# Optimization experiments

Measured on AMD Instinct MI355X. Metric: run time of the kernel, lower is better.

The kernel has to match this reference:

```python
import jax, jax.numpy as jnp
import numpy as np

N_QUBITS = 10
DIM = 2 ** N_QUBITS
W_MUL = (2.0 ** 0.5) * 5.0 ** (-0.5)  # he_std * lrmul, use_wscale=True, lrmul=1
MEASURE_QUBIT = 5


def _c(v):
    return v.astype(jnp.complex64)


def _m2(a, b, c, d):
    return jnp.stack([jnp.stack([a, b]), jnp.stack([c, d])])


_ZERO = jnp.zeros((), jnp.complex64)


def _rx(phi):
    c, s = _c(jnp.cos(phi / 2)), _c(jnp.sin(phi / 2))
    return _m2(c, -1j * s, -1j * s, c)


def _ry(phi):
    c, s = _c(jnp.cos(phi / 2)), _c(jnp.sin(phi / 2))
    return _m2(c, -s, s, c)


def _rz(phi):
    c, s = _c(jnp.cos(phi / 2)), _c(jnp.sin(phi / 2))
    return _m2(c - 1j * s, _ZERO, _ZERO, c + 1j * s)


_CNOT = jnp.array([[1, 0, 0, 0], [0, 1, 0, 0], [0, 0, 0, 1], [0, 0, 1, 0]], jnp.complex64)


def _expand(g, n, q):
    # kron(I_{2^q}, g, I_{2^{n-q-k}}) where g acts on qubits q..q+k-1
    k = int(np.log2(g.shape[0]))
    left = jnp.eye(2 ** q, dtype=jnp.complex64)
    right = jnp.eye(2 ** (n - q - k), dtype=jnp.complex64)
    return jnp.kron(left, jnp.kron(g, right))


def _layer_unitary(weight):
    w = weight * W_MUL
    U = jnp.eye(DIM, dtype=jnp.complex64)
    for sign in (1.0, -1.0):
        for q in range(N_QUBITS):
            U = _expand(_rx(sign * w[q]), N_QUBITS, q) @ U
            U = _expand(_ry(sign * w[q + 10]), N_QUBITS, q) @ U
            U = _expand(_rz(sign * w[q + 20]), N_QUBITS, q) @ U
        for q in range(1, N_QUBITS):
            U = _expand(_CNOT, N_QUBITS, q - 1) @ U
    return U


def _measure_affinity(rho, which_q):
    # Tr(rho @ Z_which_q) with Z_q = kron(I, Z, I); Z_q is diagonal
    z = jnp.array([1.0, -1.0], jnp.float32)
    zdiag = jnp.kron(jnp.ones(2 ** which_q, jnp.float32),
                     jnp.kron(z, jnp.ones(2 ** (N_QUBITS - which_q - 1), jnp.float32)))
    return jnp.sum(jnp.diagonal(rho).real * zdiag).astype(jnp.float32)


def setup_inputs() -> dict:
    key = jax.random.key(0)
    k1, k2 = jax.random.split(key)
    x = jax.random.normal(k1, (DIM, DIM), dtype=jnp.float32)
    weight = jax.random.uniform(k2, (30,), dtype=jnp.float32, minval=0.0, maxval=2.0 * np.pi)
    return {"x": x, "weight": weight}


def reference(x, weight):
    E = _layer_unitary(weight)
    rho = (E @ x.astype(jnp.complex64)) @ E.conj().T
    return _measure_affinity(rho, MEASURE_QUBIT)
```

## Files before the change

kernel.cpp:

```cpp
#include <hip/hip_runtime.h>

#define DIM 1024
#define NQ 10

__device__ __forceinline__ float2 cmul(float2 a, float2 b) {
    return make_float2(a.x * b.x - a.y * b.y, a.x * b.y + a.y * b.x);
}
__device__ __forceinline__ float2 cadd(float2 a, float2 b) {
    return make_float2(a.x + b.x, a.y + b.y);
}
__device__ __forceinline__ float2 csub(float2 a, float2 b) {
    return make_float2(a.x - b.x, a.y - b.y);
}
__device__ __forceinline__ float2 cconj(float2 a) { return make_float2(a.x, -a.y); }

__device__ __forceinline__ void mm2(const float2* A, const float2* B, float2* C) {
    C[0] = cadd(cmul(A[0], B[0]), cmul(A[1], B[2]));
    C[1] = cadd(cmul(A[0], B[1]), cmul(A[1], B[3]));
    C[2] = cadd(cmul(A[2], B[0]), cmul(A[3], B[2]));
    C[3] = cadd(cmul(A[2], B[1]), cmul(A[3], B[3]));
}

__device__ __forceinline__ void compute_gates(const float* __restrict__ weight,
                                              float2* G, float2* Msh, int tid) {
    if (tid < NQ) {
        int q = tid;
        const float WM = 0.632455532033676f;
        float px = weight[q]      * WM * 0.5f;
        float py = weight[q + 10] * WM * 0.5f;
        float pz = weight[q + 20] * WM * 0.5f;
        float cx = cosf(px), sx = sinf(px);
        float cy = cosf(py), sy = sinf(py);
        float cz = cosf(pz), sz = sinf(pz);
        {
            float2 Rx[4] = { {cx, 0.f}, {0.f, -sx}, {0.f, -sx}, {cx, 0.f} };
            float2 Ry[4] = { {cy, 0.f}, {-sy, 0.f}, {sy, 0.f}, {cy, 0.f} };
            float2 Rz[4] = { {cz, -sz}, {0.f, 0.f}, {0.f, 0.f}, {cz, sz} };
            float2 T[4], u[4];
            mm2(Ry, Rx, T);
            mm2(Rz, T, u);
            G[q * 4 + 0] = u[0]; G[q * 4 + 1] = u[1];
            G[q * 4 + 2] = u[2]; G[q * 4 + 3] = u[3];
        }
        if (Msh && q < 6) {
            float nsx = -sx, nsy = -sy, nsz = -sz;
            float2 Rx[4] = { {cx, 0.f}, {0.f, -nsx}, {0.f, -nsx}, {cx, 0.f} };
            float2 Ry[4] = { {cy, 0.f}, {-nsy, 0.f}, {nsy, 0.f}, {cy, 0.f} };
            float2 Rz[4] = { {cz, -nsz}, {0.f, 0.f}, {0.f, 0.f}, {cz, nsz} };
            float2 T[4], u2[4];
            mm2(Ry, Rx, T);
            mm2(Rz, T, u2);
            for (int i = 0; i < 2; i++)
                for (int j = 0; j < 2; j++) {
                    float2 v = csub(cmul(cconj(u2[0 * 2 + i]), u2[0 * 2 + j]),
                                    cmul(cconj(u2[1 * 2 + i]), u2[1 * 2 + j]));
                    Msh[q * 4 + i * 2 + j] = v;
                }
        }
    }
}

__global__ __launch_bounds__(512) void pass1(const float* __restrict__ x,
                                             const float* __restrict__ weight,
                                             float2* __restrict__ zt,
                                             float* __restrict__ out) {
    __shared__ float2 G[40];
    __shared__ float2 sh[DIM * 5];
    int tid = threadIdx.x;
    int lane = tid & 63;
    int w = tid >> 6;
    int rl = w >> 1;
    int h = w & 1;
    int r = blockIdx.x * 4 + rl;

    const float* xp = x + r * DIM + (h << 9) + lane;
    float2 v[8];
#pragma unroll
    for (int j = 0; j < 8; j++) v[j] = make_float2(xp[j * 64], 0.f);

    compute_gates(weight, G, nullptr, tid);
    if (blockIdx.x == 0 && tid == 0) out[0] = 0.f;
    __syncthreads();

#pragma unroll
    for (int q = 1; q < 4; q++) {
        float2 u0 = cconj(G[q * 4]),     u1 = cconj(G[q * 4 + 1]);
        float2 u2 = cconj(G[q * 4 + 2]), u3 = cconj(G[q * 4 + 3]);
        const int hb = 1 << (3 - q);
#pragma unroll
        for (int j0 = 0; j0 < 8; j0++) {
            if ((j0 & hb) == 0) {
                int j1 = j0 | hb;
                float2 s0 = v[j0], s1 = v[j1];
                v[j0] = cadd(cmul(u0, s0), cmul(u1, s1));
                v[j1] = cadd(cmul(u2, s0), cmul(u3, s1));
            }
        }
    }
#pragma unroll
    for (int q = 4; q < 10; q++) {
        float2 u0 = cconj(G[q * 4]),     u1 = cconj(G[q * 4 + 1]);
        float2 u2 = cconj(G[q * 4 + 2]), u3 = cconj(G[q * 4 + 3]);
        const int X = 1 << (9 - q);
        bool up = (lane & X) != 0;
        float2 go = up ? u3 : u0;
        float2 gp = up ? u2 : u1;
#pragma unroll
        for (int j = 0; j < 8; j++) {
            float2 p;
            p.x = __shfl_xor(v[j].x, X, 64);
            p.y = __shfl_xor(v[j].y, X, 64);
            v[j] = cadd(cmul(go, v[j]), cmul(gp, p));
        }
    }
#pragma unroll
    for (int j = 0; j < 8; j++) {
        int c = (h << 9) | (j << 6) | lane;
        sh[c * 5 + rl] = v[j];
    }
    __syncthreads();
    {
        float2 g00 = cconj(G[0]), g01 = cconj(G[1]), g10 = cconj(G[2]), g11 = cconj(G[3]);
        int cL = tid, cH = tid + 512;
        int r0 = blockIdx.x * 4;
        float2 oL[4], oH[4];
#pragma unroll
        for (int k = 0; k < 4; k++) {
            float2 L = sh[cL * 5 + k];
            float2 H = sh[cH * 5 + k];
            oL[k] = cadd(cmul(g00, L), cmul(g01, H));
            oH[k] = cadd(cmul(g10, L), cmul(g11, H));
        }
        float4* pL = (float4*)(zt + cL * DIM + r0);
        float4* pH = (float4*)(zt + cH * DIM + r0);
        pL[0] = make_float4(oL[0].x, oL[0].y, oL[1].x, oL[1].y);
        pL[1] = make_float4(oL[2].x, oL[2].y, oL[3].x, oL[3].y);
        pH[0] = make_float4(oH[0].x, oH[0].y, oH[1].x, oH[1].y);
        pH[1] = make_float4(oH[2].x, oH[2].y, oH[3].x, oH[3].y);
    }
}

__global__ __launch_bounds__(512) void pass2(const float2* __restrict__ zt,
                                             const float* __restrict__ weight,
                                             float* __restrict__ out) {
    __shared__ float2 G[40];
    __shared__ float2 Msh[24];
    __shared__ float part[8];
    int tid = threadIdx.x;
    int lane = tid & 63;
    int w = tid >> 6;
    int pr = w >> 1;
    int h = w & 1;
    int c = blockIdx.x * 4 + pr;

    const float4* zp = (const float4*)(zt + c * DIM);
    const float4* po = zp + h * 256 + lane * 4;
    const float4* pp = zp + (1 - h) * 256 + lane * 4;
    float2 a[8], b[8];
#pragma unroll
    for (int k = 0; k < 4; k++) {
        float4 t0 = po[k];
        a[2 * k]     = make_float2(t0.x, t0.y);
        a[2 * k + 1] = make_float2(t0.z, t0.w);
        float4 t1 = pp[k];
        b[2 * k]     = make_float2(t1.x, t1.y);
        b[2 * k + 1] = make_float2(t1.z, t1.w);
    }
    compute_gates(weight, G, Msh, tid);
    __syncthreads();

    float2 v[8];
    {
        float2 ga = h ? G[3] : G[0];
        float2 gb = h ? G[2] : G[1];
#pragma unroll
        for (int j = 0; j < 8; j++) v[j] = cadd(cmul(ga, a[j]), cmul(gb, b[j]));
    }
#pragma unroll
    for (int q = 1; q < 7; q++) {
        float2 u0 = G[q * 4], u1 = G[q * 4 + 1], u2 = G[q * 4 + 2], u3 = G[q * 4 + 3];
        const int X = 1 << (6 - q);
        bool up = (lane & X) != 0;
        float2 go = up ? u3 : u0;
        float2 gp = up ? u2 : u1;
#pragma unroll
        for (int j = 0; j < 8; j++) {
            float2 p;
            p.x = __shfl_xor(v[j].x, X, 64);
            p.y = __shfl_xor(v[j].y, X, 64);
            v[j] = cadd(cmul(go, v[j]), cmul(gp, p));
        }
    }
#pragma unroll
    for (int q = 7; q < 10; q++) {
        float2 u0 = G[q * 4], u1 = G[q * 4 + 1], u2 = G[q * 4 + 2], u3 = G[q * 4 + 3];
        const int hb = 1 << (9 - q);
#pragma unroll
        for (int j0 = 0; j0 < 8; j0++) {
            if ((j0 & hb) == 0) {
                int j1 = j0 | hb;
                float2 s0 = v[j0], s1 = v[j1];
                v[j0] = cadd(cmul(u0, s0), cmul(u1, s1));
                v[j1] = cadd(cmul(u2, s0), cmul(u3, s1));
            }
        }
    }

    int af = c;
    af ^= af >> 1; af ^= af >> 2; af ^= af >> 4; af ^= af >> 8;
    int t = af & 15;
    int a05 = af >> 4;
    int p5 = (lane >> 5) & 1;
    int p4 = p5 ^ ((lane >> 4) & 1);
    int p3 = p4 ^ ((lane >> 3) & 1);
    int p2 = p3 ^ ((lane >> 2) & 1);
    int p1 = p2 ^ ((lane >> 1) & 1);
    int p0 = p1 ^ (lane & 1);
    int t3 = (t >> 3) & 1, t2 = (t >> 2) & 1, t1b = (t >> 1) & 1, t0 = t & 1;
    bool sel = ((h ^ p0) == t3);
    int jsel = ((t2 ^ t3) << 2) | ((t1b ^ t2) << 1) | (t0 ^ t1b);
    float2 vs = v[0];
#pragma unroll
    for (int j = 1; j < 8; j++) if (jsel == j) vs = v[j];
    float2 m6 = make_float2(1.f, 0.f);
    int ib0 = h, ib1 = h ^ p5, ib2 = h ^ p4, ib3 = h ^ p3, ib4 = h ^ p2, ib5 = h ^ p1;
    m6 = cmul(m6, Msh[0 * 4 + ((a05 >> 5) & 1) * 2 + ib0]);
    m6 = cmul(m6, Msh[1 * 4 + ((a05 >> 4) & 1) * 2 + ib1]);
    m6 = cmul(m6, Msh[2 * 4 + ((a05 >> 3) & 1) * 2 + ib2]);
    m6 = cmul(m6, Msh[3 * 4 + ((a05 >> 2) & 1) * 2 + ib3]);
    m6 = cmul(m6, Msh[4 * 4 + ((a05 >> 1) & 1) * 2 + ib4]);
    m6 = cmul(m6, Msh[5 * 4 + (a05 & 1) * 2 + ib5]);

    float acc = sel ? (m6.x * vs.x - m6.y * vs.y) : 0.f;
#pragma unroll
    for (int off = 32; off > 0; off >>= 1) acc += __shfl_xor(acc, off, 64);
    if (lane == 0) part[w] = acc;
    __syncthreads();
    if (tid == 0) {
        float s = part[0] + part[1] + part[2] + part[3] +
                  part[4] + part[5] + part[6] + part[7];
        atomicAdd(out, s);
    }
}

extern "C" void kernel_launch(void* const* d_in, const int* in_sizes, int n_in,
                              void* d_out, int out_size, void* d_ws, size_t ws_size,
                              hipStream_t stream) {
    const float* x = (const float*)d_in[0];
    const float* weight = (const float*)d_in[1];
    float* out = (float*)d_out;

    float2* zt = (float2*)d_ws + 8192;

    pass1<<<256, 512, 0, stream>>>(x, weight, zt, out);
    pass2<<<256, 512, 0, stream>>>(zt, weight, out);
}
```

Before: 75.36 us.

## Fuse two passes into one cooperative kernel with a grid-wide sync

After: 178.0 us. 2.36x slower.

```diff
diff --git a/kernel.cpp b/kernel.cpp
--- a/kernel.cpp
+++ b/kernel.cpp
@@ -1,4 +1,7 @@
 #include <hip/hip_runtime.h>
+#include <hip/hip_cooperative_groups.h>
+
+namespace cg = cooperative_groups;
 
 #define DIM 1024
 #define NQ 10
@@ -42,7 +45,7 @@
             G[q * 4 + 0] = u[0]; G[q * 4 + 1] = u[1];
             G[q * 4 + 2] = u[2]; G[q * 4 + 3] = u[3];
         }
-        if (Msh && q < 6) {
+        if (q < 6) {
             float nsx = -sx, nsy = -sy, nsz = -sz;
             float2 Rx[4] = { {cx, 0.f}, {0.f, -nsx}, {0.f, -nsx}, {cx, 0.f} };
             float2 Ry[4] = { {cy, 0.f}, {-nsy, 0.f}, {nsy, 0.f}, {cy, 0.f} };
@@ -60,186 +63,184 @@
     }
 }
 
-__global__ __launch_bounds__(512) void pass1(const float* __restrict__ x,
+__global__ __launch_bounds__(512) void fused(const float* __restrict__ x,
                                              const float* __restrict__ weight,
                                              float2* __restrict__ zt,
                                              float* __restrict__ out) {
     __shared__ float2 G[40];
+    __shared__ float2 Msh[24];
+    __shared__ float part[8];
     __shared__ float2 sh[DIM * 5];
     int tid = threadIdx.x;
     int lane = tid & 63;
-    int w = tid >> 6;
-    int rl = w >> 1;
-    int h = w & 1;
-    int r = blockIdx.x * 4 + rl;
-
-    const float* xp = x + r * DIM + (h << 9) + lane;
-    float2 v[8];
-#pragma unroll
-    for (int j = 0; j < 8; j++) v[j] = make_float2(xp[j * 64], 0.f);
-
-    compute_gates(weight, G, nullptr, tid);
-    if (blockIdx.x == 0 && tid == 0) out[0] = 0.f;
-    __syncthreads();
-
-#pragma unroll
-    for (int q = 1; q < 4; q++) {
-        float2 u0 = cconj(G[q * 4]),     u1 = cconj(G[q * 4 + 1]);
-        float2 u2 = cconj(G[q * 4 + 2]), u3 = cconj(G[q * 4 + 3]);
-        const int hb = 1 << (3 - q);
-#pragma unroll
-        for (int j0 = 0; j0 < 8; j0++) {
-            if ((j0 & hb) == 0) {
-                int j1 = j0 | hb;
-                float2 s0 = v[j0], s1 = v[j1];
-                v[j0] = cadd(cmul(u0, s0), cmul(u1, s1));
-                v[j1] = cadd(cmul(u2, s0), cmul(u3, s1));
-            }
+    int wv = tid >> 6;
+    int h = wv & 1;
+
+    compute_gates(weight, G, Msh, tid);
+    if (blockIdx.x == 0 && tid == 0) atomicExch(out, 0.f);
+
+    {
+        int rl = wv >> 1;
+        int r = blockIdx.x * 4 + rl;
+
+        const float* xp = x + r * DIM + (h << 9) + lane;
+        float2 v[8];
+#pragma unroll
+        for (int j = 0; j < 8; j++) v[j] = make_float2(xp[j * 64], 0.f);
+
+        __syncthreads();
+
+#pragma unroll
+        for (int q = 1; q < 4; q++) {
+            float2 u0 = cconj(G[q * 4]),     u1 = cconj(G[q * 4 + 1]);
+            float2 u2 = cconj(G[q * 4 + 2]), u3 = cconj(G[q * 4 + 3]);
+            const int hb = 1 << (3 - q);
+#pragma unroll
+            for (int j0 = 0; j0 < 8; j0++) {
+                if ((j0 & hb) == 0) {
+                    int j1 = j0 | hb;
+                    float2 s0 = v[j0], s1 = v[j1];
+                    v[j0] = cadd(cmul(u0, s0), cmul(u1, s1));
+                    v[j1] = cadd(cmul(u2, s0), cmul(u3, s1));
+                }
+            }
+        }
+#pragma unroll
+        for (int q = 4; q < 10; q++) {
+            float2 u0 = cconj(G[q * 4]),     u1 = cconj(G[q * 4 + 1]);
+            float2 u2 = cconj(G[q * 4 + 2]), u3 = cconj(G[q * 4 + 3]);
+            const int X = 1 << (9 - q);
+            bool up = (lane & X) != 0;
+            float2 go = up ? u3 : u0;
+            float2 gp = up ? u2 : u1;
+#pragma unroll
+            for (int j = 0; j < 8; j++) {
+                float2 p;
+                p.x = __shfl_xor(v[j].x, X, 64);
+                p.y = __shfl_xor(v[j].y, X, 64);
+                v[j] = cadd(cmul(go, v[j]), cmul(gp, p));
+            }
+        }
+#pragma unroll
+        for (int j = 0; j < 8; j++) {
+            int c = (h << 9) | (j << 6) | lane;
+            sh[c * 5 + rl] = v[j];
+        }
+        __syncthreads();
+        {
+            float2 g00 = cconj(G[0]), g01 = cconj(G[1]), g10 = cconj(G[2]), g11 = cconj(G[3]);
+            int cL = tid, cH = tid + 512;
+            int r0 = blockIdx.x * 4;
+            float2 oL[4], oH[4];
+#pragma unroll
+            for (int k = 0; k < 4; k++) {
+                float2 L = sh[cL * 5 + k];
+                float2 H = sh[cH * 5 + k];
+                oL[k] = cadd(cmul(g00, L), cmul(g01, H));
+                oH[k] = cadd(cmul(g10, L), cmul(g11, H));
+            }
+            float4* pL = (float4*)(zt + cL * DIM + r0);
+            float4* pH = (float4*)(zt + cH * DIM + r0);
+            pL[0] = make_float4(oL[0].x, oL[0].y, oL[1].x, oL[1].y);
+            pL[1] = make_float4(oL[2].x, oL[2].y, oL[3].x, oL[3].y);
+            pH[0] = make_float4(oH[0].x, oH[0].y, oH[1].x, oH[1].y);
+            pH[1] = make_float4(oH[2].x, oH[2].y, oH[3].x, oH[3].y);
         }
     }
-#pragma unroll
-    for (int q = 4; q < 10; q++) {
-        float2 u0 = cconj(G[q * 4]),     u1 = cconj(G[q * 4 + 1]);
-        float2 u2 = cconj(G[q * 4 + 2]), u3 = cconj(G[q * 4 + 3]);
-        const int X = 1 << (9 - q);
-        bool up = (lane & X) != 0;
-        float2 go = up ? u3 : u0;
-        float2 gp = up ? u2 : u1;
-#pragma unroll
-        for (int j = 0; j < 8; j++) {
-            float2 p;
-            p.x = __shfl_xor(v[j].x, X, 64);
-            p.y = __shfl_xor(v[j].y, X, 64);
-            v[j] = cadd(cmul(go, v[j]), cmul(gp, p));
-        }
-    }
-#pragma unroll
-    for (int j = 0; j < 8; j++) {
-        int c = (h << 9) | (j << 6) | lane;
-        sh[c * 5 + rl] = v[j];
-    }
-    __syncthreads();
+
+    __threadfence();
+    cg::this_grid().sync();
+
     {
-        float2 g00 = cconj(G[0]), g01 = cconj(G[1]), g10 = cconj(G[2]), g11 = cconj(G[3]);
-        int cL = tid, cH = tid + 512;
-        int r0 = blockIdx.x * 4;
-        float2 oL[4], oH[4];
+        int pr = wv >> 1;
+        int c = blockIdx.x * 4 + pr;
+
+        const float4* zp = (const float4*)(zt + c * DIM);
+        const float4* po = zp + h * 256 + lane * 4;
+        const float4* pp = zp + (1 - h) * 256 + lane * 4;
+        float2 a[8], b[8];
 #pragma unroll
         for (int k = 0; k < 4; k++) {
-            float2 L = sh[cL * 5 + k];
-            float2 H = sh[cH * 5 + k];
-            oL[k] = cadd(cmul(g00, L), cmul(g01, H));
-            oH[k] = cadd(cmul(g10, L), cmul(g11, H));
-        }
-        float4* pL = (float4*)(zt + cL * DIM + r0);
-        float4* pH = (float4*)(zt + cH * DIM + r0);
-        pL[0] = make_float4(oL[0].x, oL[0].y, oL[1].x, oL[1].y);
-        pL[1] = make_float4(oL[2].x, oL[2].y, oL[3].x, oL[3].y);
-        pH[0] = make_float4(oH[0].x, oH[0].y, oH[1].x, oH[1].y);
-        pH[1] = make_float4(oH[2].x, oH[2].y, oH[3].x, oH[3].y);
-    }
-}
-
-__global__ __launch_bounds__(512) void pass2(const float2* __restrict__ zt,
-                                             const float* __restrict__ weight,
-                                             float* __restrict__ out) {
-    __shared__ float2 G[40];
-    __shared__ float2 Msh[24];
-    __shared__ float part[8];
-    int tid = threadIdx.x;
-    int lane = tid & 63;
-    int w = tid >> 6;
-    int pr = w >> 1;
-    int h = w & 1;
-    int c = blockIdx.x * 4 + pr;
-
-    const float4* zp = (const float4*)(zt + c * DIM);
-    const float4* po = zp + h * 256 + lane * 4;
-    const float4* pp = zp + (1 - h) * 256 + lane * 4;
-    float2 a[8], b[8];
-#pragma unroll
-    for (int k = 0; k < 4; k++) {
-        float4 t0 = po[k];
-        a[2 * k]     = make_float2(t0.x, t0.y);
-        a[2 * k + 1] = make_float2(t0.z, t0.w);
-        float4 t1 = pp[k];
-        b[2 * k]     = make_float2(t1.x, t1.y);
-        b[2 * k + 1] = make_float2(t1.z, t1.w);
-    }
-    compute_gates(weight, G, Msh, tid);
-    __syncthreads();
-
-    float2 v[8];
-    {
-        float2 ga = h ? G[3] : G[0];
-        float2 gb = h ? G[2] : G[1];
-#pragma unroll
-        for (int j = 0; j < 8; j++) v[j] = cadd(cmul(ga, a[j]), cmul(gb, b[j]));
-    }
-#pragma unroll
-    for (int q = 1; q < 7; q++) {
-        float2 u0 = G[q * 4], u1 = G[q * 4 + 1], u2 = G[q * 4 + 2], u3 = G[q * 4 + 3];
-        const int X = 1 << (6 - q);
-        bool up = (lane & X) != 0;
-        float2 go = up ? u3 : u0;
-        float2 gp = up ? u2 : u1;
-#pragma unroll
-        for (int j = 0; j < 8; j++) {
-            float2 p;
-            p.x = __shfl_xor(v[j].x, X, 64);
-            p.y = __shfl_xor(v[j].y, X, 64);
-            v[j] = cadd(cmul(go, v[j]), cmul(gp, p));
-        }
-    }
-#pragma unroll
-    for (int q = 7; q < 10; q++) {
-        float2 u0 = G[q * 4], u1 = G[q * 4 + 1], u2 = G[q * 4 + 2], u3 = G[q * 4 + 3];
-        const int hb = 1 << (9 - q);
-#pragma unroll
-        for (int j0 = 0; j0 < 8; j0++) {
-            if ((j0 & hb) == 0) {
-                int j1 = j0 | hb;
-                float2 s0 = v[j0], s1 = v[j1];
-                v[j0] = cadd(cmul(u0, s0), cmul(u1, s1));
-                v[j1] = cadd(cmul(u2, s0), cmul(u3, s1));
-            }
-        }
-    }
-
-    int af = c;
-    af ^= af >> 1; af ^= af >> 2; af ^= af >> 4; af ^= af >> 8;
-    int t = af & 15;
-    int a05 = af >> 4;
-    int p5 = (lane >> 5) & 1;
-    int p4 = p5 ^ ((lane >> 4) & 1);
-    int p3 = p4 ^ ((lane >> 3) & 1);
-    int p2 = p3 ^ ((lane >> 2) & 1);
-    int p1 = p2 ^ ((lane >> 1) & 1);
-    int p0 = p1 ^ (lane & 1);
-    int t3 = (t >> 3) & 1, t2 = (t >> 2) & 1, t1b = (t >> 1) & 1, t0 = t & 1;
-    bool sel = ((h ^ p0) == t3);
-    int jsel = ((t2 ^ t3) << 2) | ((t1b ^ t2) << 1) | (t0 ^ t1b);
-    float2 vs = v[0];
-#pragma unroll
-    for (int j = 1; j < 8; j++) if (jsel == j) vs = v[j];
-    float2 m6 = make_float2(1.f, 0.f);
-    int ib0 = h, ib1 = h ^ p5, ib2 = h ^ p4, ib3 = h ^ p3, ib4 = h ^ p2, ib5 = h ^ p1;
-    m6 = cmul(m6, Msh[0 * 4 + ((a05 >> 5) & 1) * 2 + ib0]);
-    m6 = cmul(m6, Msh[1 * 4 + ((a05 >> 4) & 1) * 2 + ib1]);
-    m6 = cmul(m6, Msh[2 * 4 + ((a05 >> 3) & 1) * 2 + ib2]);
-    m6 = cmul(m6, Msh[3 * 4 + ((a05 >> 2) & 1) * 2 + ib3]);
-    m6 = cmul(m6, Msh[4 * 4 + ((a05 >> 1) & 1) * 2 + ib4]);
-    m6 = cmul(m6, Msh[5 * 4 + (a05 & 1) * 2 + ib5]);
-
-    float acc = sel ? (m6.x * vs.x - m6.y * vs.y) : 0.f;
-#pragma unroll
-    for (int off = 32; off > 0; off >>= 1) acc += __shfl_xor(acc, off, 64);
-    if (lane == 0) part[w] = acc;
-    __syncthreads();
-    if (tid == 0) {
-        float s = part[0] + part[1] + part[2] + part[3] +
-                  part[4] + part[5] + part[6] + part[7];
-        atomicAdd(out, s);
+            float4 t0 = po[k];
+            a[2 * k]     = make_float2(t0.x, t0.y);
+            a[2 * k + 1] = make_float2(t0.z, t0.w);
+            float4 t1 = pp[k];
+            b[2 * k]     = make_float2(t1.x, t1.y);
+            b[2 * k + 1] = make_float2(t1.z, t1.w);
+        }
+
+        float2 v[8];
+        {
+            float2 ga = h ? G[3] : G[0];
+            float2 gb = h ? G[2] : G[1];
+#pragma unroll
+            for (int j = 0; j < 8; j++) v[j] = cadd(cmul(ga, a[j]), cmul(gb, b[j]));
+        }
+#pragma unroll
+        for (int q = 1; q < 7; q++) {
+            float2 u0 = G[q * 4], u1 = G[q * 4 + 1], u2 = G[q * 4 + 2], u3 = G[q * 4 + 3];
+            const int X = 1 << (6 - q);
+            bool up = (lane & X) != 0;
+            float2 go = up ? u3 : u0;
+            float2 gp = up ? u2 : u1;
+#pragma unroll
+            for (int j = 0; j < 8; j++) {
+                float2 p;
+                p.x = __shfl_xor(v[j].x, X, 64);
+                p.y = __shfl_xor(v[j].y, X, 64);
+                v[j] = cadd(cmul(go, v[j]), cmul(gp, p));
+            }
+        }
+#pragma unroll
+        for (int q = 7; q < 10; q++) {
+            float2 u0 = G[q * 4], u1 = G[q * 4 + 1], u2 = G[q * 4 + 2], u3 = G[q * 4 + 3];
+            const int hb = 1 << (9 - q);
+#pragma unroll
+            for (int j0 = 0; j0 < 8; j0++) {
+                if ((j0 & hb) == 0) {
+                    int j1 = j0 | hb;
+                    float2 s0 = v[j0], s1 = v[j1];
+                    v[j0] = cadd(cmul(u0, s0), cmul(u1, s1));
+                    v[j1] = cadd(cmul(u2, s0), cmul(u3, s1));
+                }
+            }
+        }
+
+        int af = c;
+        af ^= af >> 1; af ^= af >> 2; af ^= af >> 4; af ^= af >> 8;
+        int t = af & 15;
+        int a05 = af >> 4;
+        int p5 = (lane >> 5) & 1;
+        int p4 = p5 ^ ((lane >> 4) & 1);
+        int p3 = p4 ^ ((lane >> 3) & 1);
+        int p2 = p3 ^ ((lane >> 2) & 1);
+        int p1 = p2 ^ ((lane >> 1) & 1);
+        int p0 = p1 ^ (lane & 1);
+        int t3 = (t >> 3) & 1, t2 = (t >> 2) & 1, t1b = (t >> 1) & 1, t0 = t & 1;
+        bool sel = ((h ^ p0) == t3);
+        int jsel = ((t2 ^ t3) << 2) | ((t1b ^ t2) << 1) | (t0 ^ t1b);
+        float2 vs = v[0];
+#pragma unroll
+        for (int j = 1; j < 8; j++) if (jsel == j) vs = v[j];
+        float2 m6 = make_float2(1.f, 0.f);
+        int ib0 = h, ib1 = h ^ p5, ib2 = h ^ p4, ib3 = h ^ p3, ib4 = h ^ p2, ib5 = h ^ p1;
+        m6 = cmul(m6, Msh[0 * 4 + ((a05 >> 5) & 1) * 2 + ib0]);
+        m6 = cmul(m6, Msh[1 * 4 + ((a05 >> 4) & 1) * 2 + ib1]);
+        m6 = cmul(m6, Msh[2 * 4 + ((a05 >> 3) & 1) * 2 + ib2]);
+        m6 = cmul(m6, Msh[3 * 4 + ((a05 >> 2) & 1) * 2 + ib3]);
+        m6 = cmul(m6, Msh[4 * 4 + ((a05 >> 1) & 1) * 2 + ib4]);
+        m6 = cmul(m6, Msh[5 * 4 + (a05 & 1) * 2 + ib5]);
+
+        float acc = sel ? (m6.x * vs.x - m6.y * vs.y) : 0.f;
+#pragma unroll
+        for (int off = 32; off > 0; off >>= 1) acc += __shfl_xor(acc, off, 64);
+        if (lane == 0) part[wv] = acc;
+        __syncthreads();
+        if (tid == 0) {
+            float s = part[0] + part[1] + part[2] + part[3] +
+                      part[4] + part[5] + part[6] + part[7];
+            atomicAdd(out, s);
+        }
     }
 }
 
@@ -252,6 +253,6 @@
 
     float2* zt = (float2*)d_ws + 8192;
 
-    pass1<<<256, 512, 0, stream>>>(x, weight, zt, out);
-    pass2<<<256, 512, 0, stream>>>(zt, weight, out);
-}
+    void* args[] = { (void*)&x, (void*)&weight, (void*)&zt, (void*)&out };
+    hipLaunchCooperativeKernel((const void*)fused, dim3(256), dim3(512), args, 0, stream);
+}
```
